# Kernel tuning notes

Hardware: AMD Instinct MI355X
Metric: run time of the kernel (lower is better)

Reference implementation:

```python
import jax, jax.numpy as jnp
import numpy as np
import math

B, T, VOCAB, RANK = 32, 1024, 512, 256


def setup_inputs() -> dict:
    key = jax.random.key(0)
    k1, k2, k3, k4, k5 = jax.random.split(key, 5)
    scale_attn = 1.0 / math.sqrt(VOCAB)
    scale_proj = 1.0 / math.sqrt(RANK)
    return {
        "x": jax.random.normal(k1, (B, T, VOCAB), dtype=jnp.float32),
        "W_attn": jax.random.normal(k2, (VOCAB, 3 * RANK), dtype=jnp.float32) * scale_attn,
        "b_attn": jax.random.normal(k3, (3 * RANK,), dtype=jnp.float32) * 0.01,
        "W_proj": jax.random.normal(k4, (RANK, VOCAB), dtype=jnp.float32) * scale_proj,
        "b_proj": jax.random.normal(k5, (VOCAB,), dtype=jnp.float32) * 0.01,
    }


def reference(x, W_attn, b_attn, W_proj, b_proj):
    # x: [B, T, vocab]
    Bb, Tt, _ = x.shape
    qkv = x @ W_attn + b_attn              # [B, T, 3*rank]
    q, k, v = jnp.split(qkv, 3, axis=-1)   # each [B, T, rank]
    scale = 1.0 / math.sqrt(k.shape[-1])
    att = jnp.einsum('btd,bsd->bts', q, k) * scale  # [B, T, T]
    # causal mask (masked=True)
    mask = jnp.tril(jnp.ones((Tt, Tt), dtype=bool))
    att = jnp.where(mask[None, :, :], att, -jnp.inf)
    att = jax.nn.softmax(att, axis=-1)
    # dropout layers are identity in eval mode (p=0 attn, p=0.1 resid disabled)
    y = jnp.einsum('bts,bsd->btd', att, v)  # [B, T, rank]
    y = y @ W_proj + b_proj                 # [B, T, vocab]
    return jax.nn.gelu(y, approximate=False)
```

## Files before the change

kernel.cpp:

```cpp
#include <hip/hip_runtime.h>
#include <hip/hip_bf16.h>
#include <math.h>

typedef __bf16 bf16;
typedef __attribute__((ext_vector_type(8))) __bf16 bf16x8;
typedef __attribute__((ext_vector_type(4))) __bf16 bf16x4;
typedef __attribute__((ext_vector_type(4))) float f32x4;

#define MFMA16(a, b, c) __builtin_amdgcn_mfma_f32_16x16x32_bf16((a), (b), (c), 0, 0, 0)


__global__ __launch_bounds__(256) void cvt_wattn(const float* __restrict__ w,
                                                 bf16* __restrict__ wt) {
  int o = blockIdx.x * 256 + threadIdx.x;
  int n = o >> 9, kk = o & 511;
  wt[o] = (bf16)w[kk * 768 + n];
}

__global__ __launch_bounds__(256) void cvt_wproj(const float* __restrict__ w,
                                                 bf16* __restrict__ wt) {
  int o = blockIdx.x * 256 + threadIdx.x;
  int n = o >> 8, kk = o & 255;
  wt[o] = (bf16)w[kk * 512 + n];
}

__global__ __launch_bounds__(256) void gemm_qkv(
    const float* __restrict__ x, const bf16* __restrict__ WT,
    const float* __restrict__ b_attn,
    bf16* __restrict__ qo, bf16* __restrict__ ko, bf16* __restrict__ vto) {
  __shared__ __attribute__((aligned(16))) bf16 As[128][40];
  __shared__ __attribute__((aligned(16))) bf16 Bs[128][40];
  const int tid = threadIdx.x;
  const int id = blockIdx.x;
  const int xcd = id & 7;
  const int rest = id >> 3;
  const int bmL = rest / 6;
  const int bn = (rest % 6) * 128;
  const int bm = (xcd * 32 + bmL) * 128;
  const int lane = tid & 63, wid = tid >> 6;
  const int l15 = lane & 15, lg = lane >> 4;
  const int wm = (wid >> 1) * 64, wn = (wid & 1) * 64;

  f32x4 acc[4][4] = {};

  const int srow = tid >> 1;
  const int scol = (tid & 1) * 16;
  const float* xp = x + (size_t)(bm + srow) * 512 + scol;
  const bf16* wp = WT + (size_t)(bn + srow) * 512 + scol;

  bf16x8 ha[2], hb[2];
  {
    f32x4 f0 = *(const f32x4*)(xp);
    f32x4 f1 = *(const f32x4*)(xp + 4);
    f32x4 f2 = *(const f32x4*)(xp + 8);
    f32x4 f3 = *(const f32x4*)(xp + 12);
#pragma unroll
    for (int e = 0; e < 4; ++e) {
      ha[0][e] = (bf16)f0[e]; ha[0][e + 4] = (bf16)f1[e];
      ha[1][e] = (bf16)f2[e]; ha[1][e + 4] = (bf16)f3[e];
    }
    hb[0] = *(const bf16x8*)(wp);
    hb[1] = *(const bf16x8*)(wp + 8);
  }

  for (int kt = 0; kt < 16; ++kt) {
    __syncthreads();
    *(bf16x8*)&As[srow][scol] = ha[0];
    *(bf16x8*)&As[srow][scol + 8] = ha[1];
    *(bf16x8*)&Bs[srow][scol] = hb[0];
    *(bf16x8*)&Bs[srow][scol + 8] = hb[1];
    __syncthreads();
    if (kt < 15) {
      f32x4 f0 = *(const f32x4*)(xp + (kt + 1) * 32);
      f32x4 f1 = *(const f32x4*)(xp + (kt + 1) * 32 + 4);
      f32x4 f2 = *(const f32x4*)(xp + (kt + 1) * 32 + 8);
      f32x4 f3 = *(const f32x4*)(xp + (kt + 1) * 32 + 12);
#pragma unroll
      for (int e = 0; e < 4; ++e) {
        ha[0][e] = (bf16)f0[e]; ha[0][e + 4] = (bf16)f1[e];
        ha[1][e] = (bf16)f2[e]; ha[1][e + 4] = (bf16)f3[e];
      }
      hb[0] = *(const bf16x8*)(wp + (kt + 1) * 32);
      hb[1] = *(const bf16x8*)(wp + (kt + 1) * 32 + 8);
    }
    bf16x8 af[4], bfr[4];
#pragma unroll
    for (int mi = 0; mi < 4; ++mi)
      af[mi] = *(const bf16x8*)&As[wm + mi * 16 + l15][lg * 8];
#pragma unroll
    for (int ni = 0; ni < 4; ++ni)
      bfr[ni] = *(const bf16x8*)&Bs[wn + ni * 16 + l15][lg * 8];
    __builtin_amdgcn_s_setprio(1);
#pragma unroll
    for (int mi = 0; mi < 4; ++mi)
#pragma unroll
      for (int ni = 0; ni < 4; ++ni)
        acc[mi][ni] = MFMA16(bfr[ni], af[mi], acc[mi][ni]);
    __builtin_amdgcn_s_setprio(0);
  }

#pragma unroll
  for (int ni = 0; ni < 4; ++ni) {
    int gc0 = bn + wn + ni * 16 + lg * 4;
    f32x4 bias = *(const f32x4*)(b_attn + gc0);
    int seg = gc0 >> 8;
    int cc = gc0 & 255;
    if (seg == 2) {
#pragma unroll
      for (int mi = 0; mi < 4; ++mi) {
        int gr = bm + wm + mi * 16 + l15;
        bf16* vp = vto + (size_t)(gr >> 10) * 262144 + (size_t)cc * 1024 + (gr & 1023);
#pragma unroll
        for (int r = 0; r < 4; ++r)
          vp[(size_t)r * 1024] = (bf16)(acc[mi][ni][r] + bias[r]);
      }
    } else {
      bf16* op = (seg == 0) ? qo : ko;
#pragma unroll
      for (int mi = 0; mi < 4; ++mi) {
        int gr = bm + wm + mi * 16 + l15;
        bf16x4 pk;
#pragma unroll
        for (int r = 0; r < 4; ++r) pk[r] = (bf16)(acc[mi][ni][r] + bias[r]);
        *(bf16x4*)(op + (size_t)gr * 256 + cc) = pk;
      }
    }
  }
}

__global__ __launch_bounds__(256) void attn_fwd(
    const bf16* __restrict__ q, const bf16* __restrict__ k,
    const bf16* __restrict__ vt, bf16* __restrict__ y) {
  __shared__ __attribute__((aligned(16))) bf16 Ks[64 * 256];
  __shared__ __attribute__((aligned(16))) bf16 Vt[256 * 64];
  __shared__ __attribute__((aligned(16))) bf16 Ps[4 * 16 * 64];
  const int tid = threadIdx.x, lane = tid & 63, wid = tid >> 6;
  const int l15 = lane & 15, lg = lane >> 4;

  const int id = blockIdx.x;
  const int xcd = id & 7, u = id >> 3;
  const int bg = u & 3, j = u >> 2;
  const int b = xcd + 8 * bg;
  const int qt = (j < 8) ? j : 23 - j;
  const int q0 = qt * 64 + wid * 16;

  bf16x8 qf[8];
  {
    const bf16* qp = q + (size_t)(b * 1024 + q0 + l15) * 256 + lg * 8;
#pragma unroll
    for (int d = 0; d < 8; ++d) qf[d] = *(const bf16x8*)(qp + d * 32);
  }
  f32x4 o[16] = {};
  float m_st = -1e30f;
  float l_st = 0.f;

  const char* kbase = (const char*)(k + (size_t)b * 262144);
  const char* vtbase = (const char*)(vt + (size_t)b * 262144);
  const int ksr = tid >> 5;
  const int kscb = (tid & 31) * 16;
  const int kkey = ksr << 4;
  const int vsr = tid >> 3;
  const int vscb = (tid & 7) * 16;
  const int vkey = (vsr & 7) << 4;
  const int rkey = (l15 & 7) << 4;

  const int ntiles = qt + 1;

  bf16x8 kreg[8], vreg[8];
#pragma unroll
  for (int i = 0; i < 8; ++i)
    kreg[i] = *(const bf16x8*)(kbase + (size_t)(ksr + i * 8) * 512 + kscb);
#pragma unroll
  for (int i = 0; i < 8; ++i)
    vreg[i] = *(const bf16x8*)(vtbase + (size_t)(vsr + i * 32) * 2048 + vscb);

  for (int tt = 0; tt < ntiles; ++tt) {
    const int kv0 = tt * 64;
    __syncthreads();
#pragma unroll
    for (int i = 0; i < 8; ++i)
      *(bf16x8*)((char*)Ks + (size_t)(ksr + i * 8) * 512 + (kscb ^ kkey)) = kreg[i];
#pragma unroll
    for (int i = 0; i < 8; ++i)
      *(bf16x8*)((char*)Vt + (size_t)(vsr + i * 32) * 128 + (vscb ^ vkey)) = vreg[i];
    __syncthreads();
    if (tt + 1 < ntiles) {
      const char* kp = kbase + (size_t)(kv0 + 64) * 512;
      const char* vp = vtbase + (size_t)(kv0 + 64) * 2;
#pragma unroll
      for (int i = 0; i < 8; ++i)
        kreg[i] = *(const bf16x8*)(kp + (size_t)(ksr + i * 8) * 512 + kscb);
#pragma unroll
      for (int i = 0; i < 8; ++i)
        vreg[i] = *(const bf16x8*)(vp + (size_t)(vsr + i * 32) * 2048 + vscb);
    }

    f32x4 st[4] = {};
    __builtin_amdgcn_s_setprio(1);
#pragma unroll
    for (int nf = 0; nf < 4; ++nf) {
      const char* rp = (const char*)Ks + (size_t)(nf * 16 + l15) * 512;
#pragma unroll
      for (int dc = 0; dc < 8; ++dc) {
        bf16x8 kb = *(const bf16x8*)(rp + ((dc * 64 + lg * 16) ^ rkey));
        st[nf] = MFMA16(kb, qf[dc], st[nf]);
      }
    }
    __builtin_amdgcn_s_setprio(0);

    const int qg = q0 + l15;
    float tmax = -1e30f;
#pragma unroll
    for (int nf = 0; nf < 4; ++nf)
#pragma unroll
      for (int r = 0; r < 4; ++r) {
        int sg = kv0 + nf * 16 + lg * 4 + r;
        float v = st[nf][r] * 0.0625f;
        v = (sg > qg) ? -1e30f : v;
        st[nf][r] = v;
        tmax = fmaxf(tmax, v);
      }
    tmax = fmaxf(tmax, __shfl_xor(tmax, 16, 64));
    tmax = fmaxf(tmax, __shfl_xor(tmax, 32, 64));

    if (!__all(tmax <= m_st + 8.f)) {
      float mnew = fmaxf(m_st, tmax);
      float corr = __expf(m_st - mnew);
      m_st = mnew;
      l_st *= corr;
#pragma unroll
      for (int df = 0; df < 16; ++df)
#pragma unroll
        for (int r = 0; r < 4; ++r) o[df][r] *= corr;
    }

    char* psw = (char*)Ps + wid * 2048 + l15 * 128;
    float rsum = 0.f;
#pragma unroll
    for (int nf = 0; nf < 4; ++nf) {
      bf16x4 pk;
#pragma unroll
      for (int r = 0; r < 4; ++r) {
        float p = __expf(st[nf][r] - m_st);
        rsum += p;
        pk[r] = (bf16)p;
      }
      *(bf16x4*)(psw + ((nf * 32 + lg * 8) ^ rkey)) = pk;
    }
    rsum += __shfl_xor(rsum, 16, 64);
    rsum += __shfl_xor(rsum, 32, 64);
    l_st += rsum;

    bf16x8 pa0 = *(const bf16x8*)(psw + ((lg * 16) ^ rkey));
    bf16x8 pa1 = *(const bf16x8*)(psw + ((64 + lg * 16) ^ rkey));
    __builtin_amdgcn_s_setprio(1);
#pragma unroll
    for (int df = 0; df < 16; ++df) {
      const char* rp = (const char*)Vt + (size_t)(df * 16 + l15) * 128;
      bf16x8 vb0 = *(const bf16x8*)(rp + ((lg * 16) ^ rkey));
      bf16x8 vb1 = *(const bf16x8*)(rp + ((64 + lg * 16) ^ rkey));
      o[df] = MFMA16(vb0, pa0, o[df]);
      o[df] = MFMA16(vb1, pa1, o[df]);
    }
    __builtin_amdgcn_s_setprio(0);
  }

  float inv = 1.f / l_st;
  bf16* yp = y + (size_t)(b * 1024 + q0 + l15) * 256 + lg * 4;
#pragma unroll
  for (int df = 0; df < 16; ++df) {
    bf16x4 pk;
#pragma unroll
    for (int r = 0; r < 4; ++r) pk[r] = (bf16)(o[df][r] * inv);
    *(bf16x4*)(yp + df * 16) = pk;
  }
}

__global__ __launch_bounds__(256) void gemm_proj(
    const bf16* __restrict__ y, const bf16* __restrict__ WT,
    const float* __restrict__ b_proj, float* __restrict__ out) {
  __shared__ __attribute__((aligned(16))) bf16 As[128][40];
  __shared__ __attribute__((aligned(16))) bf16 Bs[128][40];
  const int tid = threadIdx.x;
  const int id = blockIdx.x;
  const int xcd = id & 7;
  const int rest = id >> 3;
  const int bmL = rest >> 2;
  const int bn = (rest & 3) * 128;
  const int bm = (xcd * 32 + bmL) * 128;
  const int lane = tid & 63, wid = tid >> 6;
  const int l15 = lane & 15, lg = lane >> 4;
  const int wm = (wid >> 1) * 64, wn = (wid & 1) * 64;
  f32x4 acc[4][4] = {};

  const int srow = tid >> 1, scol = (tid & 1) * 16;
  const bf16* yp = y + (size_t)(bm + srow) * 256 + scol;
  const bf16* wp = WT + (size_t)(bn + srow) * 256 + scol;

  bf16x8 ha[2], hb[2];
  ha[0] = *(const bf16x8*)(yp);
  ha[1] = *(const bf16x8*)(yp + 8);
  hb[0] = *(const bf16x8*)(wp);
  hb[1] = *(const bf16x8*)(wp + 8);

  for (int kt = 0; kt < 8; ++kt) {
    __syncthreads();
    *(bf16x8*)&As[srow][scol] = ha[0];  *(bf16x8*)&As[srow][scol + 8] = ha[1];
    *(bf16x8*)&Bs[srow][scol] = hb[0];  *(bf16x8*)&Bs[srow][scol + 8] = hb[1];
    __syncthreads();
    if (kt < 7) {
      ha[0] = *(const bf16x8*)(yp + (kt + 1) * 32);
      ha[1] = *(const bf16x8*)(yp + (kt + 1) * 32 + 8);
      hb[0] = *(const bf16x8*)(wp + (kt + 1) * 32);
      hb[1] = *(const bf16x8*)(wp + (kt + 1) * 32 + 8);
    }
    bf16x8 af[4], bfr[4];
#pragma unroll
    for (int mi = 0; mi < 4; ++mi)
      af[mi] = *(const bf16x8*)&As[wm + mi * 16 + l15][lg * 8];
#pragma unroll
    for (int ni = 0; ni < 4; ++ni)
      bfr[ni] = *(const bf16x8*)&Bs[wn + ni * 16 + l15][lg * 8];
    __builtin_amdgcn_s_setprio(1);
#pragma unroll
    for (int mi = 0; mi < 4; ++mi)
#pragma unroll
      for (int ni = 0; ni < 4; ++ni)
        acc[mi][ni] = MFMA16(bfr[ni], af[mi], acc[mi][ni]);
    __builtin_amdgcn_s_setprio(0);
  }

#pragma unroll
  for (int ni = 0; ni < 4; ++ni) {
    int gc0 = bn + wn + ni * 16 + lg * 4;
    f32x4 bias = *(const f32x4*)(b_proj + gc0);
#pragma unroll
    for (int mi = 0; mi < 4; ++mi) {
      int gr = bm + wm + mi * 16 + l15;
      f32x4 g;
#pragma unroll
      for (int r = 0; r < 4; ++r) {
        float v = acc[mi][ni][r] + bias[r];
        float z = 1.5957691216f * (v + 0.044715f * v * v * v);
        float t = __expf(z);
        float th = 1.f - 2.f / (t + 1.f);
        g[r] = 0.5f * v * (1.f + th);
      }
      *(f32x4*)(out + (size_t)gr * 512 + gc0) = g;
    }
  }
}

extern "C" void kernel_launch(void* const* d_in, const int* in_sizes, int n_in,
                              void* d_out, int out_size, void* d_ws, size_t ws_size,
                              hipStream_t stream) {
  const float* x      = (const float*)d_in[0];
  const float* W_attn = (const float*)d_in[1];
  const float* b_attn = (const float*)d_in[2];
  const float* W_proj = (const float*)d_in[3];
  const float* b_proj = (const float*)d_in[4];
  float* out = (float*)d_out;
  char* ws = (char*)d_ws;

  const size_t SZ = 16777216;
  bf16* WT1 = (bf16*)(ws);
  bf16* WT2 = (bf16*)(ws + 786432);
  bf16* qb  = (bf16*)(ws + 1048576);
  bf16* kb  = (bf16*)(ws + 1048576 + SZ);
  bf16* vtb = (bf16*)(ws + 1048576 + 2 * SZ);
  bf16* yb  = (bf16*)(ws + 1048576 + 3 * SZ);

  cvt_wattn<<<dim3(1536), dim3(256), 0, stream>>>(W_attn, WT1);
  cvt_wproj<<<dim3(512), dim3(256), 0, stream>>>(W_proj, WT2);
  gemm_qkv<<<dim3(1536), dim3(256), 0, stream>>>(x, WT1, b_attn, qb, kb, vtb);
  attn_fwd<<<dim3(512), dim3(256), 0, stream>>>(qb, kb, vtb, yb);
  gemm_proj<<<dim3(1024), dim3(256), 0, stream>>>(yb, WT2, b_proj, out);
}
```

Baseline: 135.2 us.

## Double-buffer LDS tiles in QKV and projection GEMMs with one barrier per step

Both GEMM kernels switch from a single shared-memory tile pair to two buffers. Each step reads fragments from the current buffer, stores the already-loaded next tile into the other buffer, and prefetches the tile two steps ahead into registers. This removes one of the two barriers per K step and lets LDS writes overlap MFMA work. The cost is twice the shared memory per block, which may reduce occupancy.

```diff
diff --git a/kernel.cpp b/kernel.cpp
--- a/kernel.cpp
+++ b/kernel.cpp
@@ -28,8 +28,8 @@
     const float* __restrict__ x, const bf16* __restrict__ WT,
     const float* __restrict__ b_attn,
     bf16* __restrict__ qo, bf16* __restrict__ ko, bf16* __restrict__ vto) {
-  __shared__ __attribute__((aligned(16))) bf16 As[128][40];
-  __shared__ __attribute__((aligned(16))) bf16 Bs[128][40];
+  __shared__ __attribute__((aligned(16))) bf16 As[2][128][40];
+  __shared__ __attribute__((aligned(16))) bf16 Bs[2][128][40];
   const int tid = threadIdx.x;
   const int id = blockIdx.x;
   const int xcd = id & 7;
@@ -62,34 +62,56 @@
     hb[0] = *(const bf16x8*)(wp);
     hb[1] = *(const bf16x8*)(wp + 8);
   }
-
+  *(bf16x8*)&As[0][srow][scol] = ha[0];
+  *(bf16x8*)&As[0][srow][scol + 8] = ha[1];
+  *(bf16x8*)&Bs[0][srow][scol] = hb[0];
+  *(bf16x8*)&Bs[0][srow][scol + 8] = hb[1];
+  {
+    f32x4 f0 = *(const f32x4*)(xp + 32);
+    f32x4 f1 = *(const f32x4*)(xp + 36);
+    f32x4 f2 = *(const f32x4*)(xp + 40);
+    f32x4 f3 = *(const f32x4*)(xp + 44);
+#pragma unroll
+    for (int e = 0; e < 4; ++e) {
+      ha[0][e] = (bf16)f0[e]; ha[0][e + 4] = (bf16)f1[e];
+      ha[1][e] = (bf16)f2[e]; ha[1][e + 4] = (bf16)f3[e];
+    }
+    hb[0] = *(const bf16x8*)(wp + 32);
+    hb[1] = *(const bf16x8*)(wp + 40);
+  }
+  __syncthreads();
+
+  int cur = 0;
   for (int kt = 0; kt < 16; ++kt) {
-    __syncthreads();
-    *(bf16x8*)&As[srow][scol] = ha[0];
-    *(bf16x8*)&As[srow][scol + 8] = ha[1];
-    *(bf16x8*)&Bs[srow][scol] = hb[0];
-    *(bf16x8*)&Bs[srow][scol + 8] = hb[1];
-    __syncthreads();
+    bf16x8 af[4], bfr[4];
+#pragma unroll
+    for (int mi = 0; mi < 4; ++mi)
+      af[mi] = *(const bf16x8*)&As[cur][wm + mi * 16 + l15][lg * 8];
+#pragma unroll
+    for (int ni = 0; ni < 4; ++ni)
+      bfr[ni] = *(const bf16x8*)&Bs[cur][wn + ni * 16 + l15][lg * 8];
     if (kt < 15) {
-      f32x4 f0 = *(const f32x4*)(xp + (kt + 1) * 32);
-      f32x4 f1 = *(const f32x4*)(xp + (kt + 1) * 32 + 4);
-      f32x4 f2 = *(const f32x4*)(xp + (kt + 1) * 32 + 8);
-      f32x4 f3 = *(const f32x4*)(xp + (kt + 1) * 32 + 12);
-#pragma unroll
-      for (int e = 0; e < 4; ++e) {
-        ha[0][e] = (bf16)f0[e]; ha[0][e + 4] = (bf16)f1[e];
-        ha[1][e] = (bf16)f2[e]; ha[1][e + 4] = (bf16)f3[e];
-      }
-      hb[0] = *(const bf16x8*)(wp + (kt + 1) * 32);
-      hb[1] = *(const bf16x8*)(wp + (kt + 1) * 32 + 8);
-    }
-    bf16x8 af[4], bfr[4];
-#pragma unroll
-    for (int mi = 0; mi < 4; ++mi)
-      af[mi] = *(const bf16x8*)&As[wm + mi * 16 + l15][lg * 8];
-#pragma unroll
-    for (int ni = 0; ni < 4; ++ni)
-      bfr[ni] = *(const bf16x8*)&Bs[wn + ni * 16 + l15][lg * 8];
+      const int nxt = cur ^ 1;
+      *(bf16x8*)&As[nxt][srow][scol] = ha[0];
+      *(bf16x8*)&As[nxt][srow][scol + 8] = ha[1];
+      *(bf16x8*)&Bs[nxt][srow][scol] = hb[0];
+      *(bf16x8*)&Bs[nxt][srow][scol + 8] = hb[1];
+      if (kt < 14) {
+        const float* xq = xp + (kt + 2) * 32;
+        const bf16* wq = wp + (kt + 2) * 32;
+        f32x4 f0 = *(const f32x4*)(xq);
+        f32x4 f1 = *(const f32x4*)(xq + 4);
+        f32x4 f2 = *(const f32x4*)(xq + 8);
+        f32x4 f3 = *(const f32x4*)(xq + 12);
+#pragma unroll
+        for (int e = 0; e < 4; ++e) {
+          ha[0][e] = (bf16)f0[e]; ha[0][e + 4] = (bf16)f1[e];
+          ha[1][e] = (bf16)f2[e]; ha[1][e + 4] = (bf16)f3[e];
+        }
+        hb[0] = *(const bf16x8*)(wq);
+        hb[1] = *(const bf16x8*)(wq + 8);
+      }
+    }
     __builtin_amdgcn_s_setprio(1);
 #pragma unroll
     for (int mi = 0; mi < 4; ++mi)
@@ -97,6 +119,8 @@
       for (int ni = 0; ni < 4; ++ni)
         acc[mi][ni] = MFMA16(bfr[ni], af[mi], acc[mi][ni]);
     __builtin_amdgcn_s_setprio(0);
+    __syncthreads();
+    cur ^= 1;
   }
 
 #pragma unroll
@@ -279,8 +303,8 @@
 __global__ __launch_bounds__(256) void gemm_proj(
     const bf16* __restrict__ y, const bf16* __restrict__ WT,
     const float* __restrict__ b_proj, float* __restrict__ out) {
-  __shared__ __attribute__((aligned(16))) bf16 As[128][40];
-  __shared__ __attribute__((aligned(16))) bf16 Bs[128][40];
+  __shared__ __attribute__((aligned(16))) bf16 As[2][128][40];
+  __shared__ __attribute__((aligned(16))) bf16 Bs[2][128][40];
   const int tid = threadIdx.x;
   const int id = blockIdx.x;
   const int xcd = id & 7;
@@ -302,25 +326,40 @@
   ha[1] = *(const bf16x8*)(yp + 8);
   hb[0] = *(const bf16x8*)(wp);
   hb[1] = *(const bf16x8*)(wp + 8);
-
+  *(bf16x8*)&As[0][srow][scol] = ha[0];
+  *(bf16x8*)&As[0][srow][scol + 8] = ha[1];
+  *(bf16x8*)&Bs[0][srow][scol] = hb[0];
+  *(bf16x8*)&Bs[0][srow][scol + 8] = hb[1];
+  ha[0] = *(const bf16x8*)(yp + 32);
+  ha[1] = *(const bf16x8*)(yp + 40);
+  hb[0] = *(const bf16x8*)(wp + 32);
+  hb[1] = *(const bf16x8*)(wp + 40);
+  __syncthreads();
+
+  int cur = 0;
   for (int kt = 0; kt < 8; ++kt) {
-    __syncthreads();
-    *(bf16x8*)&As[srow][scol] = ha[0];  *(bf16x8*)&As[srow][scol + 8] = ha[1];
-    *(bf16x8*)&Bs[srow][scol] = hb[0];  *(bf16x8*)&Bs[srow][scol + 8] = hb[1];
-    __syncthreads();
+    bf16x8 af[4], bfr[4];
+#pragma unroll
+    for (int mi = 0; mi < 4; ++mi)
+      af[mi] = *(const bf16x8*)&As[cur][wm + mi * 16 + l15][lg * 8];
+#pragma unroll
+    for (int ni = 0; ni < 4; ++ni)
+      bfr[ni] = *(const bf16x8*)&Bs[cur][wn + ni * 16 + l15][lg * 8];
     if (kt < 7) {
-      ha[0] = *(const bf16x8*)(yp + (kt + 1) * 32);
-      ha[1] = *(const bf16x8*)(yp + (kt + 1) * 32 + 8);
-      hb[0] = *(const bf16x8*)(wp + (kt + 1) * 32);
-      hb[1] = *(const bf16x8*)(wp + (kt + 1) * 32 + 8);
-    }
-    bf16x8 af[4], bfr[4];
-#pragma unroll
-    for (int mi = 0; mi < 4; ++mi)
-      af[mi] = *(const bf16x8*)&As[wm + mi * 16 + l15][lg * 8];
-#pragma unroll
-    for (int ni = 0; ni < 4; ++ni)
-      bfr[ni] = *(const bf16x8*)&Bs[wn + ni * 16 + l15][lg * 8];
+      const int nxt = cur ^ 1;
+      *(bf16x8*)&As[nxt][srow][scol] = ha[0];
+      *(bf16x8*)&As[nxt][srow][scol + 8] = ha[1];
+      *(bf16x8*)&Bs[nxt][srow][scol] = hb[0];
+      *(bf16x8*)&Bs[nxt][srow][scol + 8] = hb[1];
+      if (kt < 6) {
+        const bf16* yq = yp + (kt + 2) * 32;
+        const bf16* wq = wp + (kt + 2) * 32;
+        ha[0] = *(const bf16x8*)(yq);
+        ha[1] = *(const bf16x8*)(yq + 8);
+        hb[0] = *(const bf16x8*)(wq);
+        hb[1] = *(const bf16x8*)(wq + 8);
+      }
+    }
     __builtin_amdgcn_s_setprio(1);
 #pragma unroll
     for (int mi = 0; mi < 4; ++mi)
@@ -328,6 +367,8 @@
       for (int ni = 0; ni < 4; ++ni)
         acc[mi][ni] = MFMA16(bfr[ni], af[mi], acc[mi][ni]);
     __builtin_amdgcn_s_setprio(0);
+    __syncthreads();
+    cur ^= 1;
   }
 
 #pragma unroll
```

New measurement: 140.7 us. +4.1%, slower.
